# Optimization experiments

Measured on AMD Instinct MI355X. Metric: run time of the kernel, lower is better.

## Reference

```python
import jax, jax.numpy as jnp
import numpy as np

N_NODES = 50000
N_EDGES = 800000
D_IN = 512
D_OUT = 512


def setup_inputs() -> dict:
    key = jax.random.key(0)
    k1, k2, k3, k4, k5 = jax.random.split(key, 5)
    x = jax.random.normal(k1, (N_NODES, D_IN), dtype=jnp.float32)
    # DGL GraphConv weight: [in_feats, out_feats], xavier-ish scale
    weight = jax.random.normal(k2, (D_IN, D_OUT), dtype=jnp.float32) * (1.0 / np.sqrt(D_IN))
    bias = jax.random.normal(k3, (D_OUT,), dtype=jnp.float32) * 0.01
    src = jax.random.randint(k4, (N_EDGES,), 0, N_NODES, dtype=jnp.int64)
    dst = jax.random.randint(k5, (N_EDGES,), 0, N_NODES, dtype=jnp.int64)
    return {"x": x, "weight": weight, "bias": bias, "src": src, "dst": dst}


def reference(x, weight, bias, src, dst):
    # DGL GraphConv with norm='none': sum messages from src -> dst, then linear.
    # (in_feats == out_feats so DGL aggregates first, then applies W; math is
    # identical either way.)
    msgs = x[src]                                            # [E, D_IN] gather
    agg = jax.ops.segment_sum(msgs, dst, num_segments=N_NODES)  # [N, D_IN]
    return agg @ weight + bias                               # [N, D_OUT]
```

## Files before the change

kernel.cpp:

```cpp
#include <hip/hip_runtime.h>
#include <hip/hip_bf16.h>

#define NN 50000
#define NE 800000
#define DD 512
#define NPAD 50048
#define STRIDE 96

typedef __attribute__((ext_vector_type(8))) short bf16x8;
typedef __attribute__((ext_vector_type(4))) float f32x4;
typedef __attribute__((ext_vector_type(8))) unsigned short u16x8;

__device__ __align__(16) unsigned short g_Wt[DD * DD];
__device__ __align__(16) unsigned short g_xb[(size_t)NN * DD];
__device__ __align__(16) unsigned short g_agg[(size_t)NPAD * DD];
__device__ unsigned g_cnt[NN];
__device__ int g_eidx[(size_t)NN * STRIDE];

static __device__ __forceinline__ unsigned short f2bf(float f) {
    unsigned u = __float_as_uint(f);
    u += 0x7fff + ((u >> 16) & 1);
    return (unsigned short)(u >> 16);
}
static __device__ __forceinline__ float bf2f(unsigned short u) {
    return __uint_as_float((unsigned)u << 16);
}

#define FB_FILL 3125
#define FB_CONV (FB_FILL + 12500)
#define FB_WT   (FB_CONV + 1024)
#define FB_END  (FB_WT + 12)

__global__ void prep_all(const float* __restrict__ x, const float* __restrict__ W,
                         const int* __restrict__ src, const int* __restrict__ dst) {
    int b = blockIdx.x;
    int tid = threadIdx.x;
    if (b < FB_FILL) {
        int i = b * 256 + tid;
        int d = dst[i];
        unsigned pos = atomicAdd(&g_cnt[d], 1u);
        if (pos < STRIDE) g_eidx[(size_t)d * STRIDE + pos] = src[i];
    } else if (b < FB_CONV) {
        size_t base = ((size_t)(b - FB_FILL) * 256 + tid) * 8;
        f32x4 v0 = __builtin_nontemporal_load((const f32x4*)(x + base));
        f32x4 v1 = __builtin_nontemporal_load((const f32x4*)(x + base) + 1);
        u16x8 o;
        o[0] = f2bf(v0[0]); o[1] = f2bf(v0[1]); o[2] = f2bf(v0[2]); o[3] = f2bf(v0[3]);
        o[4] = f2bf(v1[0]); o[5] = f2bf(v1[1]); o[6] = f2bf(v1[2]); o[7] = f2bf(v1[3]);
        *(u16x8*)(g_xb + base) = o;
    } else if (b < FB_WT) {
        int idx = (b - FB_CONV) * 256 + tid;
        int k = idx >> 9, n = idx & 511;
        g_Wt[n * DD + k] = f2bf(W[idx]);
    } else {
        int i = (b - FB_WT) * 256 + tid;
        u16x8 z = {0, 0, 0, 0, 0, 0, 0, 0};
        *(u16x8*)(g_agg + (size_t)NN * DD + (size_t)i * 8) = z;
    }
}

__global__ void aggregate() {
    int v = (blockIdx.x * blockDim.x + threadIdx.x) >> 6;
    int lane = threadIdx.x & 63;
    if (v >= NN) return;
    int deg = (int)g_cnt[v];
    if (deg > STRIDE) deg = STRIDE;
    const int* seg = g_eidx + (size_t)v * STRIDE;
    float a[8] = {0.f, 0.f, 0.f, 0.f, 0.f, 0.f, 0.f, 0.f};
    int i = 0;
    for (; i + 1 < deg; i += 2) {
        int s0 = seg[i], s1 = seg[i + 1];
        int4 q0 = *((const int4*)(g_xb + (size_t)s0 * DD) + lane);
        int4 q1 = *((const int4*)(g_xb + (size_t)s1 * DD) + lane);
        const unsigned short* u0 = (const unsigned short*)&q0;
        const unsigned short* u1 = (const unsigned short*)&q1;
#pragma unroll
        for (int j = 0; j < 8; ++j) a[j] += bf2f(u0[j]) + bf2f(u1[j]);
    }
    if (i < deg) {
        int s0 = seg[i];
        int4 q0 = *((const int4*)(g_xb + (size_t)s0 * DD) + lane);
        const unsigned short* u0 = (const unsigned short*)&q0;
#pragma unroll
        for (int j = 0; j < 8; ++j) a[j] += bf2f(u0[j]);
    }
    u16x8 o;
#pragma unroll
    for (int j = 0; j < 8; ++j) o[j] = f2bf(a[j]);
    *(u16x8*)(g_agg + (size_t)v * DD + lane * 8) = o;
}

#define BM 128
#define BN 128
#define BK 32
#define NWG ((NPAD / BM) * (DD / BN))

__global__ __launch_bounds__(256) void gemm_kernel(float* __restrict__ out,
                                                   const float* __restrict__ bias) {
    __shared__ __align__(16) unsigned short As[BM * BK];
    __shared__ __align__(16) unsigned short Bs[BN * BK];

    const int q = NWG >> 3, r = NWG & 7;
    int xcd = blockIdx.x & 7, sub = blockIdx.x >> 3;
    int swz = (xcd < r) ? xcd * (q + 1) + sub : r * (q + 1) + (xcd - r) * q + sub;
    const int m0 = (swz >> 2) * BM;
    const int n0 = (swz & 3) * BN;

    const int tid = threadIdx.x;
    const int wave = tid >> 6, lane = tid & 63;
    const int wm = wave >> 1, wn = wave & 1;
    const int quad = lane >> 4, l16 = lane & 15;

    const int srow = lane >> 2;
    const int skoff = (lane & 3) * 8;

    f32x4 acc[4][4];
#pragma unroll
    for (int i = 0; i < 4; ++i)
#pragma unroll
        for (int j = 0; j < 4; ++j) acc[i][j] = (f32x4){0.f, 0.f, 0.f, 0.f};

    const unsigned short* gA = g_agg + (size_t)m0 * DD;
    const unsigned short* gB = g_Wt + (size_t)n0 * DD;

    for (int k0 = 0; k0 < DD; k0 += BK) {
#pragma unroll
        for (int is = 0; is < 2; ++is) {
            int row = wave * 32 + is * 16;
            __builtin_amdgcn_global_load_lds(
                (const __attribute__((address_space(1))) void*)
                    (gA + (size_t)(row + srow) * DD + k0 + skoff),
                (__attribute__((address_space(3))) void*)(As + row * BK), 16, 0, 0);
            __builtin_amdgcn_global_load_lds(
                (const __attribute__((address_space(1))) void*)
                    (gB + (size_t)(row + srow) * DD + k0 + skoff),
                (__attribute__((address_space(3))) void*)(Bs + row * BK), 16, 0, 0);
        }
        __syncthreads();

        bf16x8 af[4], bf[4];
#pragma unroll
        for (int t = 0; t < 4; ++t) {
            af[t] = *(const bf16x8*)(&As[(wm * 64 + t * 16 + l16) * BK + quad * 8]);
            bf[t] = *(const bf16x8*)(&Bs[(wn * 64 + t * 16 + l16) * BK + quad * 8]);
        }
#pragma unroll
        for (int am = 0; am < 4; ++am)
#pragma unroll
            for (int bn = 0; bn < 4; ++bn)
                acc[am][bn] = __builtin_amdgcn_mfma_f32_16x16x32_bf16(
                    af[am], bf[bn], acc[am][bn], 0, 0, 0);
        __syncthreads();
    }

#pragma unroll
    for (int am = 0; am < 4; ++am) {
        int row_base = m0 + wm * 64 + am * 16 + quad * 4;
#pragma unroll
        for (int bn = 0; bn < 4; ++bn) {
            int col = n0 + wn * 64 + bn * 16 + l16;
            float bv = bias[col];
#pragma unroll
            for (int rr = 0; rr < 4; ++rr) {
                int rowi = row_base + rr;
                if (rowi < NN) out[(size_t)rowi * DD + col] = acc[am][bn][rr] + bv;
            }
        }
    }
}

extern "C" void kernel_launch(void* const* d_in, const int* in_sizes, int n_in,
                              void* d_out, int out_size, void* d_ws, size_t ws_size,
                              hipStream_t stream) {
    const float* x    = (const float*)d_in[0];
    const float* W    = (const float*)d_in[1];
    const float* bias = (const float*)d_in[2];
    const int*   src  = (const int*)d_in[3];
    const int*   dst  = (const int*)d_in[4];
    float* out = (float*)d_out;
    (void)d_ws; (void)ws_size;

    static void* cnt_ptr = nullptr;
    if (!cnt_ptr) (void)hipGetSymbolAddress(&cnt_ptr, HIP_SYMBOL(g_cnt));
    hipMemsetAsync(cnt_ptr, 0, NN * sizeof(unsigned), stream);

    prep_all<<<FB_END, 256, 0, stream>>>(x, W, src, dst);
    aggregate<<<(NN * 64 + 255) / 256, 256, 0, stream>>>();
    gemm_kernel<<<NWG, 256, 0, stream>>>(out, bias);
}
```

Before: 406.1 us.

## Unroll gather by four, widen GEMM tile to 128x256, fold count reset into GEMM

```diff
diff --git a/kernel.cpp b/kernel.cpp
--- a/kernel.cpp
+++ b/kernel.cpp
@@ -68,10 +68,24 @@
     const int* seg = g_eidx + (size_t)v * STRIDE;
     float a[8] = {0.f, 0.f, 0.f, 0.f, 0.f, 0.f, 0.f, 0.f};
     int i = 0;
+    for (; i + 3 < deg; i += 4) {
+        int s0 = seg[i], s1 = seg[i + 1], s2 = seg[i + 2], s3 = seg[i + 3];
+        int4 q0 = *((const int4*)(g_xb + ((size_t)s0 << 9)) + lane);
+        int4 q1 = *((const int4*)(g_xb + ((size_t)s1 << 9)) + lane);
+        int4 q2 = *((const int4*)(g_xb + ((size_t)s2 << 9)) + lane);
+        int4 q3 = *((const int4*)(g_xb + ((size_t)s3 << 9)) + lane);
+        const unsigned short* u0 = (const unsigned short*)&q0;
+        const unsigned short* u1 = (const unsigned short*)&q1;
+        const unsigned short* u2 = (const unsigned short*)&q2;
+        const unsigned short* u3 = (const unsigned short*)&q3;
+#pragma unroll
+        for (int j = 0; j < 8; ++j)
+            a[j] += (bf2f(u0[j]) + bf2f(u1[j])) + (bf2f(u2[j]) + bf2f(u3[j]));
+    }
     for (; i + 1 < deg; i += 2) {
         int s0 = seg[i], s1 = seg[i + 1];
-        int4 q0 = *((const int4*)(g_xb + (size_t)s0 * DD) + lane);
-        int4 q1 = *((const int4*)(g_xb + (size_t)s1 * DD) + lane);
+        int4 q0 = *((const int4*)(g_xb + ((size_t)s0 << 9)) + lane);
+        int4 q1 = *((const int4*)(g_xb + ((size_t)s1 << 9)) + lane);
         const unsigned short* u0 = (const unsigned short*)&q0;
         const unsigned short* u1 = (const unsigned short*)&q1;
 #pragma unroll
@@ -79,7 +93,7 @@
     }
     if (i < deg) {
         int s0 = seg[i];
-        int4 q0 = *((const int4*)(g_xb + (size_t)s0 * DD) + lane);
+        int4 q0 = *((const int4*)(g_xb + ((size_t)s0 << 9)) + lane);
         const unsigned short* u0 = (const unsigned short*)&q0;
 #pragma unroll
         for (int j = 0; j < 8; ++j) a[j] += bf2f(u0[j]);
@@ -87,28 +101,33 @@
     u16x8 o;
 #pragma unroll
     for (int j = 0; j < 8; ++j) o[j] = f2bf(a[j]);
-    *(u16x8*)(g_agg + (size_t)v * DD + lane * 8) = o;
+    *(u16x8*)(g_agg + ((size_t)v << 9) + lane * 8) = o;
 }
 
 #define BM 128
-#define BN 128
+#define BN 256
 #define BK 32
 #define NWG ((NPAD / BM) * (DD / BN))
 
-__global__ __launch_bounds__(256) void gemm_kernel(float* __restrict__ out,
+__global__ __launch_bounds__(512) void gemm_kernel(float* __restrict__ out,
                                                    const float* __restrict__ bias) {
     __shared__ __align__(16) unsigned short As[BM * BK];
     __shared__ __align__(16) unsigned short Bs[BN * BK];
 
+    {
+        int gid = blockIdx.x * 512 + threadIdx.x;
+        if (gid < NN) g_cnt[gid] = 0;
+    }
+
     const int q = NWG >> 3, r = NWG & 7;
     int xcd = blockIdx.x & 7, sub = blockIdx.x >> 3;
     int swz = (xcd < r) ? xcd * (q + 1) + sub : r * (q + 1) + (xcd - r) * q + sub;
-    const int m0 = (swz >> 2) * BM;
-    const int n0 = (swz & 3) * BN;
+    const int m0 = (swz >> 1) * BM;
+    const int n0 = (swz & 1) * BN;
 
     const int tid = threadIdx.x;
     const int wave = tid >> 6, lane = tid & 63;
-    const int wm = wave >> 1, wn = wave & 1;
+    const int wm = wave >> 2, wn = wave & 3;
     const int quad = lane >> 4, l16 = lane & 15;
 
     const int srow = lane >> 2;
@@ -125,16 +144,19 @@
 
     for (int k0 = 0; k0 < DD; k0 += BK) {
 #pragma unroll
-        for (int is = 0; is < 2; ++is) {
-            int row = wave * 32 + is * 16;
-            __builtin_amdgcn_global_load_lds(
-                (const __attribute__((address_space(1))) void*)
-                    (gA + (size_t)(row + srow) * DD + k0 + skoff),
-                (__attribute__((address_space(3))) void*)(As + row * BK), 16, 0, 0);
-            __builtin_amdgcn_global_load_lds(
-                (const __attribute__((address_space(1))) void*)
-                    (gB + (size_t)(row + srow) * DD + k0 + skoff),
-                (__attribute__((address_space(3))) void*)(Bs + row * BK), 16, 0, 0);
+        for (int i = 0; i < 3; ++i) {
+            int c = wave * 3 + i;
+            if (c < 8) {
+                __builtin_amdgcn_global_load_lds(
+                    (const __attribute__((address_space(1))) void*)
+                        (gA + (size_t)(c * 16 + srow) * DD + k0 + skoff),
+                    (__attribute__((address_space(3))) void*)(As + c * 512), 16, 0, 0);
+            } else {
+                __builtin_amdgcn_global_load_lds(
+                    (const __attribute__((address_space(1))) void*)
+                        (gB + (size_t)((c - 8) * 16 + srow) * DD + k0 + skoff),
+                    (__attribute__((address_space(3))) void*)(Bs + (c - 8) * 512), 16, 0, 0);
+            }
         }
         __syncthreads();
 
@@ -180,11 +202,7 @@
     float* out = (float*)d_out;
     (void)d_ws; (void)ws_size;
 
-    static void* cnt_ptr = nullptr;
-    if (!cnt_ptr) (void)hipGetSymbolAddress(&cnt_ptr, HIP_SYMBOL(g_cnt));
-    hipMemsetAsync(cnt_ptr, 0, NN * sizeof(unsigned), stream);
-
     prep_all<<<FB_END, 256, 0, stream>>>(x, W, src, dst);
     aggregate<<<(NN * 64 + 255) / 256, 256, 0, stream>>>();
-    gemm_kernel<<<NWG, 256, 0, stream>>>(out, bias);
-}
+    gemm_kernel<<<NWG, 512, 0, stream>>>(out, bias);
+}
```

Measured after the change: 403.2 us. About the same (-0.7%).
